# Optimization experiments

Hardware: AMD Instinct MI355X
Metric: run time of the kernel (lower is better)

## Reference

```python
import jax, jax.numpy as jnp
import numpy as np

BATCH, SEQ, H, N = 8, 4096, 512, 64
DT_MIN, DT_MAX = 1e-3, 1e-1


def setup_inputs() -> dict:
    key = jax.random.key(0)
    k1, k2, k3, k4, k5 = jax.random.split(key, 5)
    n = jnp.arange(N, dtype=jnp.float32)
    # HiPPO-LegS diagonal: A[n,n] = -(n+1) -> log|diag(A)| = log(n+1)
    A_log = jnp.broadcast_to(jnp.log(n + 1.0), (H, N))
    Bv = jnp.broadcast_to(jnp.sqrt(2.0 * n + 1.0), (H, N))
    C = jax.random.normal(k1, (H, N), dtype=jnp.float32) * 0.01
    D = jnp.ones((H,), dtype=jnp.float32)
    log_dt = jax.random.uniform(k2, (H,), dtype=jnp.float32) * (
        np.log(DT_MAX) - np.log(DT_MIN)) + np.log(DT_MIN)
    # reverse-direction params (bidirectional)
    A_log_r = A_log
    B_r = Bv
    C_r = jax.random.normal(k3, (H, N), dtype=jnp.float32) * 0.01
    # out_bi Linear: weight [H, 2H], bias [H]
    W_bi = jax.random.normal(k4, (H, 2 * H), dtype=jnp.float32) / np.sqrt(2.0 * H)
    b_bi = jnp.zeros((H,), dtype=jnp.float32)
    u = jax.random.normal(k5, (BATCH, SEQ, H), dtype=jnp.float32)
    return {"u": u, "A_log": A_log, "Bv": Bv, "C": C, "D": D,
            "log_dt": log_dt, "A_log_r": A_log_r, "B_r": B_r, "C_r": C_r,
            "W_bi": W_bi, "b_bi": b_bi}


def _conv(u, A_log, Bp, Cp, D, log_dt):
    """Diagonal SSM as FFT convolution. u: [B, L, H]."""
    L = u.shape[1]
    dt = jnp.exp(log_dt)                      # [H]
    eA = jnp.exp(A_log)                       # [H, N]
    A_bar = jnp.exp(-dt[:, None] * eA)        # [H, N]
    B_bar = (A_bar - 1.0) / (-eA) * Bp        # [H, N]
    # log-space power kernel: A_bar^k = exp(k * log A_bar)
    logA = jnp.log(jnp.clip(A_bar, 1e-30, None))
    ks = jnp.arange(L, dtype=u.dtype)
    pows = jnp.exp(ks[None, None, :] * logA[:, :, None])   # [H, N, L]
    K = jnp.einsum('dn,dnl->dl', Cp * B_bar, pows)          # [H, L]
    n_fft = 2 * L
    u_f = jnp.fft.rfft(u, n=n_fft, axis=1)                  # [B, L+1, H] complex
    K_f = jnp.fft.rfft(K, n=n_fft, axis=-1)                 # [H, L+1]
    y = jnp.fft.irfft(u_f * K_f.T[None], n=n_fft, axis=1)[:, :L, :]
    return y + u * D


def reference(u, A_log, Bv, C, D, log_dt, A_log_r, B_r, C_r, W_bi, b_bi):
    y = _conv(u, A_log, Bv, C, D, log_dt)
    yr = jnp.flip(_conv(jnp.flip(u, 1), A_log_r, B_r, C_r, D, log_dt), 1)
    ycat = jnp.concatenate([y, yr], axis=-1)                # [B, L, 2H]
    return ycat @ W_bi.T + b_bi
```

## Files before the change

kernel.cpp:

```cpp
#include <hip/hip_runtime.h>
#include <hip/hip_bf16.h>
#include <stdint.h>

#define L_SEQ  4096
#define H_DIM  512
#define N_ST   64
#define N_B    8
#define N_CH   16
#define T_CH   256
#define K_GEMM 1024

typedef float  f32x4  __attribute__((ext_vector_type(4)));
typedef __bf16 bf16x8 __attribute__((ext_vector_type(8)));
typedef __bf16 bf16x4 __attribute__((ext_vector_type(4)));
typedef unsigned short u16x8 __attribute__((ext_vector_type(8)));
typedef unsigned long long ull;

#define GLOAD16(g, l) __builtin_amdgcn_global_load_lds( \
    (const __attribute__((address_space(1))) void*)(g), \
    (__attribute__((address_space(3))) void*)(l), 16, 0, 0)

__global__ __launch_bounds__(256) void k_kk(
    const float* __restrict__ A_log, const float* __restrict__ Bv,
    const float* __restrict__ C, const float* __restrict__ log_dt,
    const float* __restrict__ A_log_r, const float* __restrict__ B_r,
    const float* __restrict__ C_r,
    float* __restrict__ kk, float* __restrict__ pLG,
    float* __restrict__ pCB, float* __restrict__ pPW)
{
    __shared__ float scb[64], slg[64];
    int dirh = blockIdx.x;
    int dir  = dirh >> 9, h = dirh & 511;
    int d = threadIdx.x;
    if (d < 64) {
        int n = d;
        float dt = expf(log_dt[h]);
        const float* Al = dir ? A_log_r : A_log;
        const float* Bp = dir ? B_r    : Bv;
        const float* Cp = dir ? C_r    : C;
        float eA = expf(Al[h * N_ST + n]);
        float Ab = expf(-dt * eA);
        float Bb = (1.0f - Ab) / eA * Bp[h * N_ST + n];
        float cb = Cp[h * N_ST + n] * Bb;
        float lg = -dt * eA * 1.44269504088896f;
        scb[n] = cb; slg[n] = lg;
        pCB[dirh * 64 + n] = cb;
        pLG[dirh * 64 + n] = lg;
        pPW[dirh * 64 + n] = expf(-dt * eA * (float)T_CH);
    }
    __syncthreads();
    float s = 0.f;
    #pragma unroll
    for (int n = 0; n < 64; ++n) s += scb[n] * exp2f((float)d * slg[n]);
    kk[dirh * 256 + d] = s;
}

__global__ __launch_bounds__(256) void k_ut(
    const float* __restrict__ u, __bf16* __restrict__ ut,
    const float* __restrict__ W, __bf16* __restrict__ Wbf)
{
    __shared__ float tl[32][65];
    int blk = blockIdx.x;
    int lt = blk & 127, ht = (blk >> 7) & 7, b = blk >> 10;
    int t = threadIdx.x;
    int ho = t & 63, li = t >> 6;
    #pragma unroll
    for (int it = 0; it < 8; ++it) {
        int l = it * 4 + li;
        tl[l][ho] = u[(size_t)(b * L_SEQ + lt * 32 + l) * H_DIM + ht * 64 + ho];
    }
    if (blk < 2048) {
        int i = blk * 256 + t;
        Wbf[i] = (__bf16)W[i];
    }
    __syncthreads();
    int hh = t >> 2, lrun = (t & 3) * 8;
    bf16x8 v;
    #pragma unroll
    for (int i = 0; i < 8; ++i) v[i] = (__bf16)tl[lrun + i][hh];
    *(bf16x8*)(ut + (size_t)(ht * 64 + hh) * 32768 + b * 4096 + lt * 32 + lrun) = v;
}

__global__ __launch_bounds__(512, 2) void k_state(
    const __bf16* __restrict__ ut, const float* __restrict__ pLG,
    const float* __restrict__ pPW, __bf16* __restrict__ S2)
{
    __shared__ __bf16 uts[16384];
    int h = blockIdx.x;
    int t = threadIdx.x;
    int lane = t & 63, w = t >> 6;
    int lr = lane & 15, lg = lane >> 4;
    int dir = w >> 2, mtile = w & 3;

    float s = pLG[(size_t)(dir * 512 + h) * 64 + mtile * 16 + lr];
    f32x4 pw4 = *(const f32x4*)(pPW + (size_t)(dir * 512 + h) * 64 + mtile * 16 + lg * 4);

    bf16x8 Mf[8];
    #pragma unroll
    for (int kk = 0; kk < 8; ++kk) {
        #pragma unroll
        for (int jj = 0; jj < 8; ++jj) {
            int j = kk * 32 + lg * 8 + jj;
            float e = dir ? (float)j : (float)(255 - j);
            Mf[kk][jj] = (__bf16)exp2f(e * s);
        }
    }

    for (int hf = 0; hf < 2; ++hf) {
        if (hf) __syncthreads();
        #pragma unroll
        for (int i = 0; i < 4; ++i) {
            int chunk = i * 512 + t;
            int col   = chunk >> 5;
            int l8    = (chunk & 31) << 3;
            int l8s   = l8 ^ ((col & 7) << 3);
            GLOAD16(ut + (size_t)h * 32768 + (hf * 64 + col) * 256 + l8s,
                    (char*)uts + chunk * 16);
        }
        __syncthreads();

        #pragma unroll
        for (int ntile = 0; ntile < 4; ++ntile) {
            f32x4 acc = {};
            #pragma unroll
            for (int kk = 0; kk < 8; ++kk) {
                int col = ntile * 16 + lr;
                bf16x8 bv = *(const bf16x8*)((char*)uts + col * 512
                             + (((kk * 4 + lg) ^ (col & 7)) << 4));
                acc = __builtin_amdgcn_mfma_f32_16x16x32_bf16(Mf[kk], bv, acc, 0, 0, 0);
            }
            f32x4 X;
            if (dir == 0) {
                f32x4 incl = acc;
                float p0 = pw4[0], p1 = pw4[1], p2 = pw4[2], p3 = pw4[3];
                #pragma unroll
                for (int st = 1; st <= 8; st <<= 1) {
                    float u0 = __shfl(incl[0], (lane - st) & 63);
                    float u1 = __shfl(incl[1], (lane - st) & 63);
                    float u2 = __shfl(incl[2], (lane - st) & 63);
                    float u3 = __shfl(incl[3], (lane - st) & 63);
                    if (lr >= st) {
                        incl[0] = fmaf(p0, u0, incl[0]);
                        incl[1] = fmaf(p1, u1, incl[1]);
                        incl[2] = fmaf(p2, u2, incl[2]);
                        incl[3] = fmaf(p3, u3, incl[3]);
                    }
                    p0 *= p0; p1 *= p1; p2 *= p2; p3 *= p3;
                }
                #pragma unroll
                for (int r = 0; r < 4; ++r) {
                    float sh = __shfl(incl[r], (lane - 1) & 63);
                    X[r] = (lr == 0) ? 0.f : sh;
                }
            } else {
                f32x4 incl = acc;
                float p0 = pw4[0], p1 = pw4[1], p2 = pw4[2], p3 = pw4[3];
                #pragma unroll
                for (int st = 1; st <= 8; st <<= 1) {
                    float u0 = __shfl(incl[0], (lane + st) & 63);
                    float u1 = __shfl(incl[1], (lane + st) & 63);
                    float u2 = __shfl(incl[2], (lane + st) & 63);
                    float u3 = __shfl(incl[3], (lane + st) & 63);
                    if (lr <= 15 - st) {
                        incl[0] = fmaf(p0, u0, incl[0]);
                        incl[1] = fmaf(p1, u1, incl[1]);
                        incl[2] = fmaf(p2, u2, incl[2]);
                        incl[3] = fmaf(p3, u3, incl[3]);
                    }
                    p0 *= p0; p1 *= p1; p2 *= p2; p3 *= p3;
                }
                #pragma unroll
                for (int r = 0; r < 4; ++r) {
                    float sh = __shfl(incl[r], (lane + 1) & 63);
                    X[r] = (lr == 15) ? 0.f : sh;
                }
            }
            int colg = hf * 64 + ntile * 16 + lr;
            int nq   = mtile * 4 + lg;
            bf16x4 o;
            #pragma unroll
            for (int r = 0; r < 4; ++r) o[r] = (__bf16)X[r];
            *(bf16x4*)(S2 + ((size_t)((dir * 512 + h) * 16 + nq) * 128 + colg) * 4) = o;
        }
    }
}

template<int DIR>
__device__ __forceinline__ void conv_body(
    int h, int t,
    const float* __restrict__ kk, const float* __restrict__ pLG,
    const float* __restrict__ pCB, const float* __restrict__ Dv,
    const __bf16* __restrict__ ut, const __bf16* __restrict__ S,
    __bf16* __restrict__ ycT,
    __bf16* uts, ull* kkq8, float* slg, float* scb)
{
    int dirh = DIR * 512 + h;
    int lane = t & 63, w = t >> 6;
    int lr = lane & 15, lg = lane >> 4;

    unsigned short* asc = (unsigned short*)uts;
    for (int i = t; i < 548; i += 512) {
        int d = DIR ? (i - 272) : (271 - i);
        float kv = (d >= 0 && d < 256) ? kk[dirh * 256 + d] : 0.f;
        asc[i] = __builtin_bit_cast(unsigned short, (__bf16)kv);
    }
    if (t < 64)       slg[t]      = pLG[dirh * 64 + t];
    else if (t < 128) scb[t - 64] = pCB[dirh * 64 + (t - 64)];
    __syncthreads();
    for (int i = t; i < 544; i += 512)
        kkq8[i] = (ull)asc[i] | ((ull)asc[i+1] << 16) | ((ull)asc[i+2] << 32)
                | ((ull)asc[i+3] << 48);
    __syncthreads();

    bf16x8 gvv[2][2];
    #pragma unroll
    for (int nt = 0; nt < 2; ++nt)
        #pragma unroll
        for (int mf = 0; mf < 2; ++mf) {
            int rt = mf ? (15 - w) : w;
            int l  = rt * 16 + lr;
            float e = DIR ? (float)(256 - l) : (float)(l + 1);
            #pragma unroll
            for (int j = 0; j < 8; ++j) {
                int n = nt * 32 + lg * 8 + j;
                gvv[nt][mf][j] = (__bf16)(scb[n] * exp2f(e * slg[n]));
            }
        }

    float Dh = Dv[h];
    const ull* kq = kkq8;

    for (int hf = 0; hf < 2; ++hf) {
        #pragma unroll
        for (int i = 0; i < 4; ++i) {
            int chunk = i * 512 + t;
            int col   = chunk >> 5;
            int l8    = (chunk & 31) << 3;
            int l8s   = l8 ^ ((col & 7) << 3);
            GLOAD16(ut + (size_t)h * 32768 + (hf * 64 + col) * 256 + l8s,
                    (char*)uts + chunk * 16);
        }
        __syncthreads();

        f32x4 acc[2][4] = {};

        #pragma unroll
        for (int mf = 0; mf < 2; ++mf) {
            int rt  = mf ? (15 - w) : w;
            int jlo = DIR ? (rt >> 1) : 0;
            int jhi = DIR ? 8 : ((rt >> 1) + 1);
            int sb  = (DIR ? 272 : 271) + lg * 8 - rt * 16 - lr;
            for (int jt = jlo; jt < jhi; ++jt) {
                bf16x8 bv[4];
                #pragma unroll
                for (int n = 0; n < 4; ++n) {
                    int col = n * 16 + lr;
                    bv[n] = *(const bf16x8*)((char*)uts + col * 512
                              + (((jt * 4 + lg) ^ (col & 7)) << 4));
                }
                int si = sb + jt * 32;
                ull lo = kq[si], hi = kq[si + 4];
                bf16x8 av;
                ((ull*)&av)[0] = lo; ((ull*)&av)[1] = hi;
                #pragma unroll
                for (int n = 0; n < 4; ++n)
                    acc[mf][n] = __builtin_amdgcn_mfma_f32_16x16x32_bf16(av, bv[n], acc[mf][n], 0, 0, 0);
            }
        }

        #pragma unroll
        for (int nt = 0; nt < 2; ++nt) {
            bf16x8 bs[4];
            #pragma unroll
            for (int n = 0; n < 4; ++n) {
                int colg = (hf * 4 + n) * 16 + lr;
                int nq0  = nt * 8 + lg * 2;
                const __bf16* sp = S + ((size_t)((DIR * 512 + h) * 16 + nq0) * 128 + colg) * 4;
                bf16x4 s0 = *(const bf16x4*)(sp);
                bf16x4 s1 = *(const bf16x4*)(sp + 512);
                #pragma unroll
                for (int j = 0; j < 4; ++j) { bs[n][j] = s0[j]; bs[n][4 + j] = s1[j]; }
            }
            #pragma unroll
            for (int mf = 0; mf < 2; ++mf)
                #pragma unroll
                for (int n = 0; n < 4; ++n)
                    acc[mf][n] = __builtin_amdgcn_mfma_f32_16x16x32_bf16(gvv[nt][mf], bs[n], acc[mf][n], 0, 0, 0);
        }

        #pragma unroll
        for (int mf = 0; mf < 2; ++mf) {
            int rt = mf ? (15 - w) : w;
            int l0 = rt * 16 + lg * 4;
            #pragma unroll
            for (int n = 0; n < 4; ++n) {
                int col = n * 16 + lr;
                bf16x4 uv = *(const bf16x4*)((char*)uts + col * 512
                             + ((((l0 >> 3) ^ (col & 7)) << 4) | ((l0 & 7) * 2)));
                bf16x4 o;
                #pragma unroll
                for (int r = 0; r < 4; ++r)
                    o[r] = (__bf16)(acc[mf][n][r] + Dh * (float)uv[r]);
                *(bf16x4*)(ycT + (size_t)dirh * 32768 + (hf * 64 + col) * 256 + l0) = o;
            }
        }
        __syncthreads();
    }
}

__global__ __launch_bounds__(512, 4) void k_conv(
    const float* __restrict__ kk, const float* __restrict__ pLG,
    const float* __restrict__ pCB, const float* __restrict__ Dv,
    const __bf16* __restrict__ ut, const __bf16* __restrict__ S,
    __bf16* __restrict__ ycT)
{
    __shared__ __bf16 uts[16384];
    __shared__ ull kkq8[544];
    __shared__ float slg[64], scb[64];
    int h = blockIdx.x & 511;
    int t = threadIdx.x;
    if (blockIdx.x >> 9)
        conv_body<1>(h, t, kk, pLG, pCB, Dv, ut, S, ycT, uts, kkq8, slg, scb);
    else
        conv_body<0>(h, t, kk, pLG, pCB, Dv, ut, S, ycT, uts, kkq8, slg, scb);
}

__global__ __launch_bounds__(256, 2) void k_gemm(
    const __bf16* __restrict__ ycT, const __bf16* __restrict__ B,
    const float* __restrict__ bias, float* __restrict__ out)
{
    __shared__ __bf16 As[2][4][128][8];
    __shared__ __bf16 Bs[2][256][32];
    int t  = threadIdx.x;
    int l  = t & 63, w = t >> 6;
    int lr = l & 15, lg = l >> 4;
    int mBase = blockIdx.y * 128;
    int nBase = blockIdx.x * 256;
    int wr = (w >> 1) * 64, wc = (w & 1) * 128;

    int sT  = t & 15;
    int sp  = t >> 4;
    int swz  = (sT & 7) << 4;
    int kgrp = sp >> 2;
    int keb  = (sp & 3) * 4;

    f32x4 acc[4][8] = {};
    const __bf16* aptr = ycT + mBase + sT * 8;

#define STAGE_A(buf, va0, va1) do { \
    char* AsB_ = (char*)&As[buf][0][0][0]; \
    _Pragma("unroll") \
    for (int i = 0; i < 8; ++i) { \
        unsigned v_ = (unsigned)(unsigned short)(va0)[i] \
                    | ((unsigned)(unsigned short)(va1)[i] << 16); \
        int off_ = ((kgrp * 128 + sT * 8 + i) * 16 + keb) ^ swz; \
        *(unsigned*)(AsB_ + off_) = v_; \
    } } while (0)

#define STAGE_B(buf, kt_) do { \
    char* BsB_ = (char*)&Bs[buf][0][0]; \
    _Pragma("unroll") \
    for (int i = 0; i < 4; ++i) { \
        int chunk_ = i * 256 + t; \
        int row_ = chunk_ >> 2, kq_ = chunk_ & 3; \
        int kqs_ = kq_ ^ ((row_ >> 1) & 3); \
        GLOAD16(B + (size_t)(nBase + row_) * K_GEMM + (kt_) + kqs_ * 8, \
                BsB_ + chunk_ * 16); \
    } } while (0)

#define COMPUTE(buf) do { \
    char* AsB_ = (char*)&As[buf][0][0][0]; \
    char* BsB_ = (char*)&Bs[buf][0][0]; \
    bf16x8 af_[4], bfv_[8]; \
    _Pragma("unroll") \
    for (int m = 0; m < 4; ++m) { \
        int row_ = wr + m * 16 + lr; \
        int off_ = ((lg * 128 + row_) * 16) ^ (((row_ >> 3) & 7) << 4); \
        af_[m] = *(const bf16x8*)(AsB_ + off_); \
    } \
    _Pragma("unroll") \
    for (int n = 0; n < 8; ++n) { \
        int row_ = wc + n * 16 + lr; \
        bfv_[n] = *(const bf16x8*)(BsB_ + row_ * 64 \
                    + ((lg * 16) ^ (((row_ >> 1) & 3) << 4))); \
    } \
    _Pragma("unroll") \
    for (int m = 0; m < 4; ++m) \
        _Pragma("unroll") \
        for (int n = 0; n < 8; ++n) \
            acc[m][n] = __builtin_amdgcn_mfma_f32_16x16x32_bf16(af_[m], bfv_[n], acc[m][n], 0, 0, 0); \
    } while (0)

    u16x8 a0 = *(const u16x8*)(aptr + (size_t)(2 * sp) * 32768);
    u16x8 a1 = *(const u16x8*)(aptr + (size_t)(2 * sp + 1) * 32768);
    STAGE_A(0, a0, a1);
    STAGE_B(0, 0);
    asm volatile("s_waitcnt vmcnt(0)" ::: "memory");
    __builtin_amdgcn_sched_barrier(0);
    a0 = *(const u16x8*)(aptr + (size_t)(32 + 2 * sp) * 32768);
    a1 = *(const u16x8*)(aptr + (size_t)(32 + 2 * sp + 1) * 32768);
    __builtin_amdgcn_sched_barrier(0);
    asm volatile("s_waitcnt lgkmcnt(0)" ::: "memory");
    __builtin_amdgcn_s_barrier();

    int cur = 0;
    for (int kt = 0; kt < K_GEMM - 32; kt += 32) {
        int nxt = cur ^ 1;
        STAGE_A(nxt, a0, a1);
        STAGE_B(nxt, kt + 32);
        COMPUTE(cur);
        asm volatile("s_waitcnt vmcnt(0)" ::: "memory");
        __builtin_amdgcn_sched_barrier(0);
        if (kt + 64 < K_GEMM) {
            a0 = *(const u16x8*)(aptr + (size_t)(kt + 64 + 2 * sp) * 32768);
            a1 = *(const u16x8*)(aptr + (size_t)(kt + 64 + 2 * sp + 1) * 32768);
        }
        __builtin_amdgcn_sched_barrier(0);
        asm volatile("s_waitcnt lgkmcnt(0)" ::: "memory");
        __builtin_amdgcn_s_barrier();
        cur = nxt;
    }
    COMPUTE(cur);

#undef STAGE_A
#undef STAGE_B
#undef COMPUTE

    #pragma unroll
    for (int n = 0; n < 8; ++n) {
        int colg = nBase + wc + n * 16 + lr;
        float bv = bias[colg];
        #pragma unroll
        for (int m = 0; m < 4; ++m) {
            int rowg = mBase + wr + m * 16 + lg * 4;
            #pragma unroll
            for (int r = 0; r < 4; ++r)
                out[(size_t)(rowg + r) * H_DIM + colg] = acc[m][n][r] + bv;
        }
    }
}

extern "C" void kernel_launch(void* const* d_in, const int* in_sizes, int n_in,
                              void* d_out, int out_size, void* d_ws, size_t ws_size,
                              hipStream_t stream)
{
    const float* u       = (const float*)d_in[0];
    const float* A_log   = (const float*)d_in[1];
    const float* Bv      = (const float*)d_in[2];
    const float* C       = (const float*)d_in[3];
    const float* D       = (const float*)d_in[4];
    const float* log_dt  = (const float*)d_in[5];
    const float* A_log_r = (const float*)d_in[6];
    const float* B_r     = (const float*)d_in[7];
    const float* C_r     = (const float*)d_in[8];
    const float* W_bi    = (const float*)d_in[9];
    const float* b_bi    = (const float*)d_in[10];
    float* out = (float*)d_out;

    char* ws = (char*)d_ws;
    float* pCB  = (float*)(ws + 0x040000);
    float* pPW  = (float*)(ws + 0x080000);
    float* pLG  = (float*)(ws + 0x0C0000);
    float* kk   = (float*)(ws + 0x100000);
    __bf16* Wbf = (__bf16*)(ws + 0x200000);
    __bf16* S   = (__bf16*)(ws + 0x300000);
    __bf16* ut  = (__bf16*)(ws + 0x1300000);
    __bf16* ycT = (__bf16*)(ws + 0x3300000);

    k_kk   <<<1024, 256, 0, stream>>>(A_log, Bv, C, log_dt, A_log_r, B_r, C_r,
                                      kk, pLG, pCB, pPW);
    k_ut   <<<8192, 256, 0, stream>>>(u, ut, W_bi, Wbf);
    k_state<<<512,  512, 0, stream>>>(ut, pLG, pPW, S);
    k_conv <<<1024, 512, 0, stream>>>(kk, pLG, pCB, D, ut, S, ycT);
    dim3 g(2, 256);
    k_gemm <<<g,    256, 0, stream>>>(ycT, Wbf, b_bi, out);
}
```

Before: 137.7 us.

## Prefetch both u halves in conv; shrink GEMM tile to single-buffered 128x128

In the conv kernel, both halves of the u tile are loaded into a doubled LDS buffer up front. A partial vmcnt wait lets compute on the first half start while the second half is still loading, and the trailing barrier is dropped. The GEMM kernel moves from a double-buffered 128x256 tile to a single-buffered 128x128 tile with twice as many blocks and a higher occupancy hint. This trades software pipelining for more blocks and less LDS per block, and adds a second barrier on every k-step.

```diff
diff --git a/kernel.cpp b/kernel.cpp
--- a/kernel.cpp
+++ b/kernel.cpp
@@ -230,7 +230,8 @@
     float Dh = Dv[h];
     const ull* kq = kkq8;
 
-    for (int hf = 0; hf < 2; ++hf) {
+    #pragma unroll
+    for (int hf = 0; hf < 2; ++hf)
         #pragma unroll
         for (int i = 0; i < 4; ++i) {
             int chunk = i * 512 + t;
@@ -238,9 +239,17 @@
             int l8    = (chunk & 31) << 3;
             int l8s   = l8 ^ ((col & 7) << 3);
             GLOAD16(ut + (size_t)h * 32768 + (hf * 64 + col) * 256 + l8s,
-                    (char*)uts + chunk * 16);
-        }
-        __syncthreads();
+                    (char*)uts + hf * 32768 + chunk * 16);
+        }
+    asm volatile("s_waitcnt vmcnt(4)" ::: "memory");
+    __builtin_amdgcn_sched_barrier(0);
+    __builtin_amdgcn_s_barrier();
+    __builtin_amdgcn_sched_barrier(0);
+
+    #pragma unroll
+    for (int hf = 0; hf < 2; ++hf) {
+        if (hf) __syncthreads();
+        char* ub = (char*)uts + hf * 32768;
 
         f32x4 acc[2][4] = {};
 
@@ -255,7 +264,7 @@
                 #pragma unroll
                 for (int n = 0; n < 4; ++n) {
                     int col = n * 16 + lr;
-                    bv[n] = *(const bf16x8*)((char*)uts + col * 512
+                    bv[n] = *(const bf16x8*)(ub + col * 512
                               + (((jt * 4 + lg) ^ (col & 7)) << 4));
                 }
                 int si = sb + jt * 32;
@@ -295,7 +304,7 @@
             #pragma unroll
             for (int n = 0; n < 4; ++n) {
                 int col = n * 16 + lr;
-                bf16x4 uv = *(const bf16x4*)((char*)uts + col * 512
+                bf16x4 uv = *(const bf16x4*)(ub + col * 512
                              + ((((l0 >> 3) ^ (col & 7)) << 4) | ((l0 & 7) * 2)));
                 bf16x4 o;
                 #pragma unroll
@@ -304,7 +313,6 @@
                 *(bf16x4*)(ycT + (size_t)dirh * 32768 + (hf * 64 + col) * 256 + l0) = o;
             }
         }
-        __syncthreads();
     }
 }
 
@@ -314,7 +322,7 @@
     const __bf16* __restrict__ ut, const __bf16* __restrict__ S,
     __bf16* __restrict__ ycT)
 {
-    __shared__ __bf16 uts[16384];
+    __shared__ __bf16 uts[32768];
     __shared__ ull kkq8[544];
     __shared__ float slg[64], scb[64];
     int h = blockIdx.x & 511;
@@ -325,18 +333,18 @@
         conv_body<0>(h, t, kk, pLG, pCB, Dv, ut, S, ycT, uts, kkq8, slg, scb);
 }
 
-__global__ __launch_bounds__(256, 2) void k_gemm(
+__global__ __launch_bounds__(256, 3) void k_gemm(
     const __bf16* __restrict__ ycT, const __bf16* __restrict__ B,
     const float* __restrict__ bias, float* __restrict__ out)
 {
-    __shared__ __bf16 As[2][4][128][8];
-    __shared__ __bf16 Bs[2][256][32];
+    __shared__ __bf16 As[4][128][8];
+    __shared__ __bf16 Bs[128][32];
     int t  = threadIdx.x;
     int l  = t & 63, w = t >> 6;
     int lr = l & 15, lg = l >> 4;
     int mBase = blockIdx.y * 128;
-    int nBase = blockIdx.x * 256;
-    int wr = (w >> 1) * 64, wc = (w & 1) * 128;
+    int nBase = blockIdx.x * 128;
+    int wr = (w >> 1) * 64, wc = (w & 1) * 64;
 
     int sT  = t & 15;
     int sp  = t >> 4;
@@ -344,90 +352,58 @@
     int kgrp = sp >> 2;
     int keb  = (sp & 3) * 4;
 
-    f32x4 acc[4][8] = {};
+    char* AsB = (char*)&As[0][0][0];
+    char* BsB = (char*)&Bs[0][0];
+    f32x4 acc[4][4] = {};
     const __bf16* aptr = ycT + mBase + sT * 8;
-
-#define STAGE_A(buf, va0, va1) do { \
-    char* AsB_ = (char*)&As[buf][0][0][0]; \
-    _Pragma("unroll") \
-    for (int i = 0; i < 8; ++i) { \
-        unsigned v_ = (unsigned)(unsigned short)(va0)[i] \
-                    | ((unsigned)(unsigned short)(va1)[i] << 16); \
-        int off_ = ((kgrp * 128 + sT * 8 + i) * 16 + keb) ^ swz; \
-        *(unsigned*)(AsB_ + off_) = v_; \
-    } } while (0)
-
-#define STAGE_B(buf, kt_) do { \
-    char* BsB_ = (char*)&Bs[buf][0][0]; \
-    _Pragma("unroll") \
-    for (int i = 0; i < 4; ++i) { \
-        int chunk_ = i * 256 + t; \
-        int row_ = chunk_ >> 2, kq_ = chunk_ & 3; \
-        int kqs_ = kq_ ^ ((row_ >> 1) & 3); \
-        GLOAD16(B + (size_t)(nBase + row_) * K_GEMM + (kt_) + kqs_ * 8, \
-                BsB_ + chunk_ * 16); \
-    } } while (0)
-
-#define COMPUTE(buf) do { \
-    char* AsB_ = (char*)&As[buf][0][0][0]; \
-    char* BsB_ = (char*)&Bs[buf][0][0]; \
-    bf16x8 af_[4], bfv_[8]; \
-    _Pragma("unroll") \
-    for (int m = 0; m < 4; ++m) { \
-        int row_ = wr + m * 16 + lr; \
-        int off_ = ((lg * 128 + row_) * 16) ^ (((row_ >> 3) & 7) << 4); \
-        af_[m] = *(const bf16x8*)(AsB_ + off_); \
-    } \
-    _Pragma("unroll") \
-    for (int n = 0; n < 8; ++n) { \
-        int row_ = wc + n * 16 + lr; \
-        bfv_[n] = *(const bf16x8*)(BsB_ + row_ * 64 \
-                    + ((lg * 16) ^ (((row_ >> 1) & 3) << 4))); \
-    } \
-    _Pragma("unroll") \
-    for (int m = 0; m < 4; ++m) \
-        _Pragma("unroll") \
-        for (int n = 0; n < 8; ++n) \
-            acc[m][n] = __builtin_amdgcn_mfma_f32_16x16x32_bf16(af_[m], bfv_[n], acc[m][n], 0, 0, 0); \
-    } while (0)
 
     u16x8 a0 = *(const u16x8*)(aptr + (size_t)(2 * sp) * 32768);
     u16x8 a1 = *(const u16x8*)(aptr + (size_t)(2 * sp + 1) * 32768);
-    STAGE_A(0, a0, a1);
-    STAGE_B(0, 0);
-    asm volatile("s_waitcnt vmcnt(0)" ::: "memory");
-    __builtin_amdgcn_sched_barrier(0);
-    a0 = *(const u16x8*)(aptr + (size_t)(32 + 2 * sp) * 32768);
-    a1 = *(const u16x8*)(aptr + (size_t)(32 + 2 * sp + 1) * 32768);
-    __builtin_amdgcn_sched_barrier(0);
-    asm volatile("s_waitcnt lgkmcnt(0)" ::: "memory");
-    __builtin_amdgcn_s_barrier();
-
-    int cur = 0;
-    for (int kt = 0; kt < K_GEMM - 32; kt += 32) {
-        int nxt = cur ^ 1;
-        STAGE_A(nxt, a0, a1);
-        STAGE_B(nxt, kt + 32);
-        COMPUTE(cur);
-        asm volatile("s_waitcnt vmcnt(0)" ::: "memory");
-        __builtin_amdgcn_sched_barrier(0);
-        if (kt + 64 < K_GEMM) {
-            a0 = *(const u16x8*)(aptr + (size_t)(kt + 64 + 2 * sp) * 32768);
-            a1 = *(const u16x8*)(aptr + (size_t)(kt + 64 + 2 * sp + 1) * 32768);
-        }
-        __builtin_amdgcn_sched_barrier(0);
-        asm volatile("s_waitcnt lgkmcnt(0)" ::: "memory");
-        __builtin_amdgcn_s_barrier();
-        cur = nxt;
-    }
-    COMPUTE(cur);
-
-#undef STAGE_A
-#undef STAGE_B
-#undef COMPUTE
-
-    #pragma unroll
-    for (int n = 0; n < 8; ++n) {
+
+    for (int kt = 0; kt < K_GEMM; kt += 32) {
+        __syncthreads();
+        #pragma unroll
+        for (int i = 0; i < 8; ++i) {
+            unsigned v = (unsigned)(unsigned short)a0[i]
+                       | ((unsigned)(unsigned short)a1[i] << 16);
+            int off = ((kgrp * 128 + sT * 8 + i) * 16 + keb) ^ swz;
+            *(unsigned*)(AsB + off) = v;
+        }
+        #pragma unroll
+        for (int i = 0; i < 2; ++i) {
+            int chunk = i * 256 + t;
+            int row = chunk >> 2, kq = chunk & 3;
+            int kqs = kq ^ ((row >> 1) & 3);
+            GLOAD16(B + (size_t)(nBase + row) * K_GEMM + kt + kqs * 8,
+                    BsB + chunk * 16);
+        }
+        __syncthreads();
+        if (kt + 32 < K_GEMM) {
+            a0 = *(const u16x8*)(aptr + (size_t)(kt + 32 + 2 * sp) * 32768);
+            a1 = *(const u16x8*)(aptr + (size_t)(kt + 32 + 2 * sp + 1) * 32768);
+        }
+        bf16x8 af[4], bfv[4];
+        #pragma unroll
+        for (int m = 0; m < 4; ++m) {
+            int row = wr + m * 16 + lr;
+            int off = ((lg * 128 + row) * 16) ^ (((row >> 3) & 7) << 4);
+            af[m] = *(const bf16x8*)(AsB + off);
+        }
+        #pragma unroll
+        for (int n = 0; n < 4; ++n) {
+            int row = wc + n * 16 + lr;
+            bfv[n] = *(const bf16x8*)(BsB + row * 64
+                       + ((lg * 16) ^ (((row >> 1) & 3) << 4)));
+        }
+        #pragma unroll
+        for (int m = 0; m < 4; ++m)
+            #pragma unroll
+            for (int n = 0; n < 4; ++n)
+                acc[m][n] = __builtin_amdgcn_mfma_f32_16x16x32_bf16(af[m], bfv[n], acc[m][n], 0, 0, 0);
+    }
+
+    #pragma unroll
+    for (int n = 0; n < 4; ++n) {
         int colg = nBase + wc + n * 16 + lr;
         float bv = bias[colg];
         #pragma unroll
@@ -472,6 +448,6 @@
     k_ut   <<<8192, 256, 0, stream>>>(u, ut, W_bi, Wbf);
     k_state<<<512,  512, 0, stream>>>(ut, pLG, pPW, S);
     k_conv <<<1024, 512, 0, stream>>>(kk, pLG, pCB, D, ut, S, ycT);
-    dim3 g(2, 256);
+    dim3 g(4, 256);
     k_gemm <<<g,    256, 0, stream>>>(ycT, Wbf, b_bi, out);
 }
```

Measured after the change: 138.7 us. Within noise of the previous version (+0.7%).

## Prefetch both u halves into LDS and restructure GEMM staging pipeline

Applied to the files above, without the earlier changes.

In the conv kernel, both halves of the transposed input tile are loaded into a doubled LDS buffer up front. The second half's load can then overlap compute on the first, and one of the two barriers per half goes away. In the GEMM, the A and B staging order changes: A is staged into the current buffer just before compute, with the next global load issued early and a partial vmcnt wait. The goal is to hide global-load latency. Doubling LDS in k_conv (64KB for uts) may reduce occupancy below the launch-bound target of 4 blocks.

```diff
diff --git a/kernel.cpp b/kernel.cpp
--- a/kernel.cpp
+++ b/kernel.cpp
@@ -230,7 +230,8 @@
     float Dh = Dv[h];
     const ull* kq = kkq8;
 
-    for (int hf = 0; hf < 2; ++hf) {
+    #pragma unroll
+    for (int hf = 0; hf < 2; ++hf)
         #pragma unroll
         for (int i = 0; i < 4; ++i) {
             int chunk = i * 512 + t;
@@ -238,9 +239,17 @@
             int l8    = (chunk & 31) << 3;
             int l8s   = l8 ^ ((col & 7) << 3);
             GLOAD16(ut + (size_t)h * 32768 + (hf * 64 + col) * 256 + l8s,
-                    (char*)uts + chunk * 16);
-        }
-        __syncthreads();
+                    (char*)uts + hf * 32768 + chunk * 16);
+        }
+    asm volatile("s_waitcnt vmcnt(4)" ::: "memory");
+    __builtin_amdgcn_sched_barrier(0);
+    __builtin_amdgcn_s_barrier();
+    __builtin_amdgcn_sched_barrier(0);
+
+    #pragma unroll
+    for (int hf = 0; hf < 2; ++hf) {
+        if (hf) __syncthreads();
+        char* ub = (char*)uts + hf * 32768;
 
         f32x4 acc[2][4] = {};
 
@@ -255,7 +264,7 @@
                 #pragma unroll
                 for (int n = 0; n < 4; ++n) {
                     int col = n * 16 + lr;
-                    bv[n] = *(const bf16x8*)((char*)uts + col * 512
+                    bv[n] = *(const bf16x8*)(ub + col * 512
                               + (((jt * 4 + lg) ^ (col & 7)) << 4));
                 }
                 int si = sb + jt * 32;
@@ -295,7 +304,7 @@
             #pragma unroll
             for (int n = 0; n < 4; ++n) {
                 int col = n * 16 + lr;
-                bf16x4 uv = *(const bf16x4*)((char*)uts + col * 512
+                bf16x4 uv = *(const bf16x4*)(ub + col * 512
                              + ((((l0 >> 3) ^ (col & 7)) << 4) | ((l0 & 7) * 2)));
                 bf16x4 o;
                 #pragma unroll
@@ -304,7 +313,6 @@
                 *(bf16x4*)(ycT + (size_t)dirh * 32768 + (hf * 64 + col) * 256 + l0) = o;
             }
         }
-        __syncthreads();
     }
 }
 
@@ -314,7 +322,7 @@
     const __bf16* __restrict__ ut, const __bf16* __restrict__ S,
     __bf16* __restrict__ ycT)
 {
-    __shared__ __bf16 uts[16384];
+    __shared__ __bf16 uts[32768];
     __shared__ ull kkq8[544];
     __shared__ float slg[64], scb[64];
     int h = blockIdx.x & 511;
@@ -393,33 +401,28 @@
 
     u16x8 a0 = *(const u16x8*)(aptr + (size_t)(2 * sp) * 32768);
     u16x8 a1 = *(const u16x8*)(aptr + (size_t)(2 * sp + 1) * 32768);
-    STAGE_A(0, a0, a1);
     STAGE_B(0, 0);
-    asm volatile("s_waitcnt vmcnt(0)" ::: "memory");
-    __builtin_amdgcn_sched_barrier(0);
-    a0 = *(const u16x8*)(aptr + (size_t)(32 + 2 * sp) * 32768);
-    a1 = *(const u16x8*)(aptr + (size_t)(32 + 2 * sp + 1) * 32768);
-    __builtin_amdgcn_sched_barrier(0);
-    asm volatile("s_waitcnt lgkmcnt(0)" ::: "memory");
-    __builtin_amdgcn_s_barrier();
 
     int cur = 0;
     for (int kt = 0; kt < K_GEMM - 32; kt += 32) {
         int nxt = cur ^ 1;
-        STAGE_A(nxt, a0, a1);
+        STAGE_A(cur, a0, a1);
+        a0 = *(const u16x8*)(aptr + (size_t)(kt + 32 + 2 * sp) * 32768);
+        a1 = *(const u16x8*)(aptr + (size_t)(kt + 32 + 2 * sp + 1) * 32768);
         STAGE_B(nxt, kt + 32);
+        asm volatile("s_waitcnt vmcnt(6) lgkmcnt(0)" ::: "memory");
+        __builtin_amdgcn_sched_barrier(0);
+        __builtin_amdgcn_s_barrier();
+        __builtin_amdgcn_sched_barrier(0);
         COMPUTE(cur);
-        asm volatile("s_waitcnt vmcnt(0)" ::: "memory");
-        __builtin_amdgcn_sched_barrier(0);
-        if (kt + 64 < K_GEMM) {
-            a0 = *(const u16x8*)(aptr + (size_t)(kt + 64 + 2 * sp) * 32768);
-            a1 = *(const u16x8*)(aptr + (size_t)(kt + 64 + 2 * sp + 1) * 32768);
-        }
-        __builtin_amdgcn_sched_barrier(0);
-        asm volatile("s_waitcnt lgkmcnt(0)" ::: "memory");
         __builtin_amdgcn_s_barrier();
-        cur = nxt;
-    }
+        cur ^= 1;
+    }
+    STAGE_A(cur, a0, a1);
+    asm volatile("s_waitcnt vmcnt(0) lgkmcnt(0)" ::: "memory");
+    __builtin_amdgcn_sched_barrier(0);
+    __builtin_amdgcn_s_barrier();
+    __builtin_amdgcn_sched_barrier(0);
     COMPUTE(cur);
 
 #undef STAGE_A
```

New measurement: 131.0 us. -4.9%, faster.
